# Optimization experiments

Hardware: AMD Instinct MI355X
Metric: run time of the kernel (lower is better)

Reference implementation:

```python
import jax, jax.numpy as jnp
import numpy as np

B, F_IN, F_OUT, D, K = 32, 64, 64, 512, 64


def setup_inputs() -> dict:
    key = jax.random.key(0)
    k1, k2, k3 = jax.random.split(key, 3)
    x = jax.random.normal(k1, (B, F_IN, D), dtype=jnp.float32)
    # Evaluated monomial-word operators: K matrices of size D x D
    word_ops = jax.random.normal(k2, (K, D, D), dtype=jnp.float32)
    # nn.init.uniform_ -> U[0,1)
    coeff = jax.random.uniform(k3, (F_OUT, F_IN, K), dtype=jnp.float32)
    return {"x": x, "word_ops": word_ops, "coeff": coeff}


def reference(x, word_ops, coeff):
    # Per sample in the torch code:
    #   evals[i, d, k] = (X @ W_k)[i, d] = sum_e X[i, e] * W[k, e, d]
    #   res = tensordot(coeff, evals, ([1, 2], [0, 2]))  -> [F_out, D]
    # Fully batched fused contraction (replaces the Python loop over batch):
    # evals: [B, F_in, D, K]
    evals = jnp.einsum('bie,ked->bidk', x, word_ops)
    # out: [B, F_out, D]
    out = jnp.einsum('oik,bidk->bod', coeff, evals)
    return out
```

## Files before the change

### kernel.cpp

```cpp
#include <hip/hip_runtime.h>


#define KK 32768

typedef __attribute__((ext_vector_type(8))) short bf16x8;
typedef __attribute__((ext_vector_type(4))) float f32x4;

__device__ __forceinline__ unsigned short f2bf(float f) {
  unsigned int u = __float_as_uint(f);
  return (unsigned short)((u + 0x7FFFu + ((u >> 16) & 1u)) >> 16);
}

__device__ __forceinline__ void gld16(void* lds, const void* g) {
  __builtin_amdgcn_global_load_lds((const __attribute__((address_space(1))) void*)g,
                                   (__attribute__((address_space(3))) void*)lds,
                                   16, 0, 0);
}

__global__ __launch_bounds__(256) void convW(const float* __restrict__ W,
                                             unsigned short* __restrict__ WbT) {
  __shared__ float tile[64][65];
  int bx = blockIdx.x;
  int k = bx >> 6, et = (bx >> 3) & 7, dt = bx & 7;
  int t = threadIdx.x;
  const float* src = W + ((size_t)k * 512 + (size_t)et * 64) * 512 + dt * 64;
  int rr = t >> 6, cc = t & 63;
#pragma unroll
  for (int p = 0; p < 16; p++) {
    int e = p * 4 + rr;
    tile[e][cc] = src[(size_t)e * 512 + cc];
  }
  __syncthreads();
  int dl = t >> 4, eg = t & 15;
#pragma unroll
  for (int p = 0; p < 4; p++) {
    int d = p * 16 + dl;
    ushort4 v;
    v.x = f2bf(tile[eg * 4 + 0][d]);
    v.y = f2bf(tile[eg * 4 + 1][d]);
    v.z = f2bf(tile[eg * 4 + 2][d]);
    v.w = f2bf(tile[eg * 4 + 3][d]);
    *(ushort4*)(WbT + (size_t)(dt * 64 + d) * KK + k * 512 + et * 64 + eg * 4) = v;
  }
}

__global__ __launch_bounds__(256) void convX(const float* __restrict__ x,
                                             unsigned short* __restrict__ xT) {
  __shared__ unsigned short lds[64 * 130];
  int bx = blockIdx.x;
  int b = bx >> 2, ec = bx & 3;
  int t = threadIdx.x;
  const float* src = x + (size_t)b * 32768 + ec * 128;
#pragma unroll
  for (int j = 0; j < 32; j++) {
    int idx = j * 256 + t;
    int i = idx >> 7, e = idx & 127;
    lds[i * 130 + e] = f2bf(src[(size_t)i * 512 + e]);
  }
  __syncthreads();
  unsigned short* dst = xT + (size_t)b * 32768 + ec * 128 * 64;
#pragma unroll
  for (int j = 0; j < 32; j++) {
    int idx = j * 256 + t;
    int e = idx >> 6, i = idx & 63;
    dst[idx] = lds[i * 130 + e];
  }
}

__global__ __launch_bounds__(256) void convC(const float* __restrict__ c,
                                             unsigned short* __restrict__ cb) {
  __shared__ unsigned short lds[64 * 66];
  int rb = blockIdx.x;
  int t = threadIdx.x;
  const float* src = c + (size_t)rb * 4096;
#pragma unroll
  for (int j = 0; j < 16; j++) {
    int idx = j * 256 + t;
    int r = idx >> 6, k = idx & 63;
    lds[r * 66 + k] = f2bf(src[idx]);
  }
  __syncthreads();
#pragma unroll
  for (int j = 0; j < 16; j++) {
    int idx = j * 256 + t;
    int k = idx >> 6, r = idx & 63;
    cb[(size_t)k * 4096 + rb * 64 + r] = lds[r * 66 + k];
  }
}

__global__ __launch_bounds__(256, 2) void tkern(const unsigned short* __restrict__ xT,
                                                const unsigned short* __restrict__ cb,
                                                unsigned short* __restrict__ Tb) {
  __shared__ unsigned short xe[128 * 64];
  __shared__ unsigned short ck[4 * 64 * 64];
  __shared__ unsigned short ot[64 * 132];
  int bx = blockIdx.x;
  int eq = bx & 3, kq = (bx >> 2) & 15, b = bx >> 6;
  int t = threadIdx.x;
  {
    const unsigned short* gx = xT + (size_t)b * 32768 + (size_t)eq * 8192;
#pragma unroll
    for (int j = 0; j < 4; j++) {
      int idx = j * 256 + t;
      int e = idx >> 3, cg = (idx & 7) ^ (e & 7);
      gld16((char*)xe + idx * 16, gx + e * 64 + cg * 8);
    }
    const unsigned short* gc = cb + (size_t)(kq * 4) * 4096;
#pragma unroll
    for (int j = 0; j < 8; j++) {
      int idx = j * 256 + t;
      int row = idx >> 3, cg = (idx & 7) ^ (row & 7);
      gld16((char*)ck + idx * 16, gc + row * 64 + cg * 8);
    }
  }
  __syncthreads();
  int wid = t >> 6, lane = t & 63, q = lane >> 4, l16 = lane & 15;
  bf16x8 ax[2][2];
#pragma unroll
  for (int ef = 0; ef < 2; ef++)
#pragma unroll
    for (int ks2 = 0; ks2 < 2; ks2++) {
      int e = wid * 32 + ef * 16 + l16;
      int s2 = (ks2 * 4 + q) ^ (e & 7);
      ax[ef][ks2] = *(const bf16x8*)(xe + e * 64 + s2 * 8);
    }
  size_t mbase = (size_t)(b * 64);
#pragma unroll 1
  for (int kj = 0; kj < 4; kj++) {
    const unsigned short* ckk = ck + kj * 4096;
    bf16x8 bc[4][2];
#pragma unroll
    for (int of = 0; of < 4; of++)
#pragma unroll
      for (int ks2 = 0; ks2 < 2; ks2++) {
        int o = of * 16 + l16;
        int s2 = (ks2 * 4 + q) ^ (o & 7);
        bc[of][ks2] = *(const bf16x8*)(ckk + o * 64 + s2 * 8);
      }
    f32x4 acc[2][4] = {};
#pragma unroll
    for (int ef = 0; ef < 2; ef++)
#pragma unroll
      for (int of = 0; of < 4; of++)
#pragma unroll
        for (int ks2 = 0; ks2 < 2; ks2++)
          acc[ef][of] = __builtin_amdgcn_mfma_f32_16x16x32_bf16(ax[ef][ks2], bc[of][ks2],
                                                                acc[ef][of], 0, 0, 0);
    __syncthreads();
#pragma unroll
    for (int ef = 0; ef < 2; ef++)
#pragma unroll
      for (int of = 0; of < 4; of++) {
        int o = of * 16 + l16;
        int e = wid * 32 + ef * 16 + q * 4;
        ushort4 v;
        v.x = f2bf(acc[ef][of][0]);
        v.y = f2bf(acc[ef][of][1]);
        v.z = f2bf(acc[ef][of][2]);
        v.w = f2bf(acc[ef][of][3]);
        *(ushort4*)(ot + o * 132 + e) = v;
      }
    __syncthreads();
    unsigned short* gdst = Tb + mbase * KK + (size_t)(kq * 4 + kj) * 512 + eq * 128;
#pragma unroll
    for (int j = 0; j < 8; j++) {
      int idx = j * 256 + t;
      int o = idx >> 5, c = idx & 31;
      *(ushort4*)(gdst + (size_t)o * KK + c * 4) = *(const ushort4*)(ot + o * 132 + c * 4);
    }
  }
}

__global__ __launch_bounds__(256, 4) void gemm_kern(const unsigned short* __restrict__ A,
                                                    const unsigned short* __restrict__ Bt,
                                                    float* __restrict__ out) {
  __shared__ unsigned short As[128 * 64];
  __shared__ unsigned short Bs[128 * 64];
  int bx = blockIdx.x;
  int ks = bx & 15, nt = (bx >> 4) & 3, mt = bx >> 6;
  int m0 = mt * 128, n0 = nt * 128, k0 = ks * 2048;
  int t = threadIdx.x;
  int wid = t >> 6, lane = t & 63, q = lane >> 4, l16 = lane & 15;
  int wm = (wid & 1) * 64, wn = (wid >> 1) * 64;
  f32x4 acc[4][4] = {};
  int srow = t >> 3;
  int cg = (t & 7) ^ (srow & 7);
  const char* gabase = (const char*)(A + (size_t)m0 * KK + k0) + (size_t)srow * 65536 + cg * 16;
  const char* gbbase = (const char*)(Bt + (size_t)n0 * KK + k0) + (size_t)srow * 65536 + cg * 16;
  int sw0 = q ^ (l16 & 7);
  int sw1 = (4 | q) ^ (l16 & 7);
#pragma unroll 1
  for (int kc = 0; kc < 2048; kc += 64) {
    const char* ga = gabase + (size_t)kc * 2;
    const char* gb = gbbase + (size_t)kc * 2;
#pragma unroll
    for (int j = 0; j < 4; j++) {
      gld16((char*)As + (j * 256 + t) * 16, ga + (size_t)j * 32 * 65536);
      gld16((char*)Bs + (j * 256 + t) * 16, gb + (size_t)j * 32 * 65536);
    }
    __syncthreads();
#pragma unroll
    for (int ks2 = 0; ks2 < 2; ks2++) {
      int slot = ks2 ? sw1 : sw0;
      bf16x8 af[4], bfr[4];
#pragma unroll
      for (int fr = 0; fr < 4; fr++)
        af[fr] = *(const bf16x8*)(As + (wm + fr * 16 + l16) * 64 + slot * 8);
#pragma unroll
      for (int fc = 0; fc < 4; fc++)
        bfr[fc] = *(const bf16x8*)(Bs + (wn + fc * 16 + l16) * 64 + slot * 8);
#pragma unroll
      for (int fr = 0; fr < 4; fr++)
#pragma unroll
        for (int fc = 0; fc < 4; fc++)
          acc[fr][fc] = __builtin_amdgcn_mfma_f32_16x16x32_bf16(af[fr], bfr[fc], acc[fr][fc], 0, 0, 0);
    }
    __syncthreads();
  }
#pragma unroll
  for (int fr = 0; fr < 4; fr++)
#pragma unroll
    for (int fc = 0; fc < 4; fc++)
#pragma unroll
      for (int r = 0; r < 4; r++)
        atomicAdd(&out[(size_t)(m0 + wm + fr * 16 + q * 4 + r) * 512 + n0 + wn + fc * 16 + l16],
                  acc[fr][fc][r]);
}

__global__ __launch_bounds__(256) void fallback_kern(const float* __restrict__ x,
                                                     const float* __restrict__ W,
                                                     const float* __restrict__ coeff,
                                                     float* __restrict__ out) {
  __shared__ float ev[64][129];
  int b = blockIdx.x >> 6, k = blockIdx.x & 63;
  int t = threadIdx.x, dl = t & 127, half = t >> 7;
  const float* xb = x + (size_t)b * 64 * 512;
  const float* Wk = W + (size_t)k * 512 * 512;
  for (int dc = 0; dc < 4; dc++) {
    int d = dc * 128 + dl;
    for (int i = half * 32; i < half * 32 + 32; i++) {
      float acc = 0.f;
      const float* xr = xb + (size_t)i * 512;
#pragma unroll 4
      for (int e = 0; e < 512; e++) acc += xr[e] * Wk[(size_t)e * 512 + d];
      ev[i][dl] = acc;
    }
    __syncthreads();
    for (int o = half * 32; o < half * 32 + 32; o++) {
      float s = 0.f;
#pragma unroll 8
      for (int i = 0; i < 64; i++) s += coeff[((size_t)o * 64 + i) * 64 + k] * ev[i][dl];
      atomicAdd(&out[((size_t)(b * 64 + o)) * 512 + d], s);
    }
    __syncthreads();
  }
}

extern "C" void kernel_launch(void* const* d_in, const int* in_sizes, int n_in,
                              void* d_out, int out_size, void* d_ws, size_t ws_size,
                              hipStream_t stream) {
  const float* x = (const float*)d_in[0];
  const float* W = (const float*)d_in[1];
  const float* coeff = (const float*)d_in[2];
  float* out = (float*)d_out;
  const size_t OFF_XT = 33554432;
  const size_t OFF_CB = OFF_XT + 2097152;
  const size_t OFF_TB = OFF_CB + 524288;
  const size_t NEED = OFF_TB + 134217728;

  hipMemsetAsync(d_out, 0, (size_t)out_size * sizeof(float), stream);
  if (ws_size >= NEED) {
    unsigned short* WbT = (unsigned short*)d_ws;
    unsigned short* xT  = (unsigned short*)((char*)d_ws + OFF_XT);
    unsigned short* cb  = (unsigned short*)((char*)d_ws + OFF_CB);
    unsigned short* Tb  = (unsigned short*)((char*)d_ws + OFF_TB);
    convX<<<128, 256, 0, stream>>>(x, xT);
    convC<<<64, 256, 0, stream>>>(coeff, cb);
    convW<<<4096, 256, 0, stream>>>(W, WbT);
    tkern<<<2048, 256, 0, stream>>>(xT, cb, Tb);
    gemm_kern<<<1024, 256, 0, stream>>>(Tb, WbT, out);
  } else {
    fallback_kern<<<2048, 256, 0, stream>>>(x, W, coeff, out);
  }
}
```

Baseline: 246.9 us.

## Double-buffer coeff tiles in tkern, shrink LDS, merge convX/convC launches

The tkern kernel no longer loads all four coefficient slices into LDS up front. It double-buffers one 64x64 slice at a time, prefetching the next slice while computing the current one. The output staging buffer now alternates with the x tile's LDS region, which is free once x has been read into registers. That removes one barrier per iteration and cuts the LDS footprint, so occupancy goes from 2 to 3 blocks. convX and convC are also merged into one launch to save a kernel launch. The cost is more fragile aliasing and synchronisation reasoning.

```diff
diff --git a/kernel.cpp b/kernel.cpp
--- a/kernel.cpp
+++ b/kernel.cpp
@@ -44,56 +44,56 @@
   }
 }
 
-__global__ __launch_bounds__(256) void convX(const float* __restrict__ x,
-                                             unsigned short* __restrict__ xT) {
+__global__ __launch_bounds__(256) void convXC(const float* __restrict__ x,
+                                              const float* __restrict__ c,
+                                              unsigned short* __restrict__ xT,
+                                              unsigned short* __restrict__ cb) {
   __shared__ unsigned short lds[64 * 130];
-  int bx = blockIdx.x;
-  int b = bx >> 2, ec = bx & 3;
-  int t = threadIdx.x;
-  const float* src = x + (size_t)b * 32768 + ec * 128;
-#pragma unroll
-  for (int j = 0; j < 32; j++) {
-    int idx = j * 256 + t;
-    int i = idx >> 7, e = idx & 127;
-    lds[i * 130 + e] = f2bf(src[(size_t)i * 512 + e]);
-  }
-  __syncthreads();
-  unsigned short* dst = xT + (size_t)b * 32768 + ec * 128 * 64;
-#pragma unroll
-  for (int j = 0; j < 32; j++) {
-    int idx = j * 256 + t;
-    int e = idx >> 6, i = idx & 63;
-    dst[idx] = lds[i * 130 + e];
-  }
-}
-
-__global__ __launch_bounds__(256) void convC(const float* __restrict__ c,
-                                             unsigned short* __restrict__ cb) {
-  __shared__ unsigned short lds[64 * 66];
-  int rb = blockIdx.x;
-  int t = threadIdx.x;
-  const float* src = c + (size_t)rb * 4096;
-#pragma unroll
-  for (int j = 0; j < 16; j++) {
-    int idx = j * 256 + t;
-    int r = idx >> 6, k = idx & 63;
-    lds[r * 66 + k] = f2bf(src[idx]);
-  }
-  __syncthreads();
-#pragma unroll
-  for (int j = 0; j < 16; j++) {
-    int idx = j * 256 + t;
-    int k = idx >> 6, r = idx & 63;
-    cb[(size_t)k * 4096 + rb * 64 + r] = lds[r * 66 + k];
-  }
-}
-
-__global__ __launch_bounds__(256, 2) void tkern(const unsigned short* __restrict__ xT,
+  int t = threadIdx.x;
+  if (blockIdx.x < 128) {
+    int bx = blockIdx.x;
+    int b = bx >> 2, ec = bx & 3;
+    const float* src = x + (size_t)b * 32768 + ec * 128;
+#pragma unroll
+    for (int j = 0; j < 32; j++) {
+      int idx = j * 256 + t;
+      int i = idx >> 7, e = idx & 127;
+      lds[i * 130 + e] = f2bf(src[(size_t)i * 512 + e]);
+    }
+    __syncthreads();
+    unsigned short* dst = xT + (size_t)b * 32768 + ec * 128 * 64;
+#pragma unroll
+    for (int j = 0; j < 32; j++) {
+      int idx = j * 256 + t;
+      int e = idx >> 6, i = idx & 63;
+      dst[idx] = lds[i * 130 + e];
+    }
+  } else {
+    int rb = blockIdx.x - 128;
+    const float* src = c + (size_t)rb * 4096;
+#pragma unroll
+    for (int j = 0; j < 16; j++) {
+      int idx = j * 256 + t;
+      int r = idx >> 6, k = idx & 63;
+      lds[r * 66 + k] = f2bf(src[idx]);
+    }
+    __syncthreads();
+#pragma unroll
+    for (int j = 0; j < 16; j++) {
+      int idx = j * 256 + t;
+      int k = idx >> 6, r = idx & 63;
+      cb[(size_t)k * 4096 + rb * 64 + r] = lds[r * 66 + k];
+    }
+  }
+}
+
+__global__ __launch_bounds__(256, 3) void tkern(const unsigned short* __restrict__ xT,
                                                 const unsigned short* __restrict__ cb,
                                                 unsigned short* __restrict__ Tb) {
-  __shared__ unsigned short xe[128 * 64];
-  __shared__ unsigned short ck[4 * 64 * 64];
-  __shared__ unsigned short ot[64 * 132];
+  __shared__ unsigned short u0[64 * 132];
+  __shared__ unsigned short ck[2][64 * 64];
+  __shared__ unsigned short ot0[64 * 132];
+  unsigned short* xe = u0;
   int bx = blockIdx.x;
   int eq = bx & 3, kq = (bx >> 2) & 15, b = bx >> 6;
   int t = threadIdx.x;
@@ -107,10 +107,10 @@
     }
     const unsigned short* gc = cb + (size_t)(kq * 4) * 4096;
 #pragma unroll
-    for (int j = 0; j < 8; j++) {
-      int idx = j * 256 + t;
-      int row = idx >> 3, cg = (idx & 7) ^ (row & 7);
-      gld16((char*)ck + idx * 16, gc + row * 64 + cg * 8);
+    for (int j = 0; j < 2; j++) {
+      int idx = j * 256 + t;
+      int o = idx >> 3, cg = (idx & 7) ^ (o & 7);
+      gld16((char*)ck[0] + idx * 16, gc + o * 64 + cg * 8);
     }
   }
   __syncthreads();
@@ -127,7 +127,17 @@
   size_t mbase = (size_t)(b * 64);
 #pragma unroll 1
   for (int kj = 0; kj < 4; kj++) {
-    const unsigned short* ckk = ck + kj * 4096;
+    int cur = kj & 1;
+    if (kj < 3) {
+      const unsigned short* gc = cb + (size_t)(kq * 4 + kj + 1) * 4096;
+#pragma unroll
+      for (int j = 0; j < 2; j++) {
+        int idx = j * 256 + t;
+        int o = idx >> 3, cg = (idx & 7) ^ (o & 7);
+        gld16((char*)ck[cur ^ 1] + idx * 16, gc + o * 64 + cg * 8);
+      }
+    }
+    const unsigned short* ckk = ck[cur];
     bf16x8 bc[4][2];
 #pragma unroll
     for (int of = 0; of < 4; of++)
@@ -146,7 +156,7 @@
         for (int ks2 = 0; ks2 < 2; ks2++)
           acc[ef][of] = __builtin_amdgcn_mfma_f32_16x16x32_bf16(ax[ef][ks2], bc[of][ks2],
                                                                 acc[ef][of], 0, 0, 0);
-    __syncthreads();
+    unsigned short* ot = cur ? u0 : ot0;
 #pragma unroll
     for (int ef = 0; ef < 2; ef++)
 #pragma unroll
@@ -165,8 +175,8 @@
 #pragma unroll
     for (int j = 0; j < 8; j++) {
       int idx = j * 256 + t;
-      int o = idx >> 5, c = idx & 31;
-      *(ushort4*)(gdst + (size_t)o * KK + c * 4) = *(const ushort4*)(ot + o * 132 + c * 4);
+      int o = idx >> 5, cc2 = idx & 31;
+      *(ushort4*)(gdst + (size_t)o * KK + cc2 * 4) = *(const ushort4*)(ot + o * 132 + cc2 * 4);
     }
   }
 }
@@ -274,8 +284,7 @@
     unsigned short* xT  = (unsigned short*)((char*)d_ws + OFF_XT);
     unsigned short* cb  = (unsigned short*)((char*)d_ws + OFF_CB);
     unsigned short* Tb  = (unsigned short*)((char*)d_ws + OFF_TB);
-    convX<<<128, 256, 0, stream>>>(x, xT);
-    convC<<<64, 256, 0, stream>>>(coeff, cb);
+    convXC<<<192, 256, 0, stream>>>(x, coeff, xT, cb);
     convW<<<4096, 256, 0, stream>>>(W, WbT);
     tkern<<<2048, 256, 0, stream>>>(xT, cb, Tb);
     gemm_kern<<<1024, 256, 0, stream>>>(Tb, WbT, out);
```

New measurement: 240.3 us. -2.7%, faster.
